# Kernel optimization log

Hardware: AMD Instinct MI355X
Metric: run time of the kernel (lower is better)

Reference implementation:

```python
import jax, jax.numpy as jnp
import numpy as np

D_MODEL = 768
N_HEADS = 12
HEAD_DIM = D_MODEL // N_HEADS
D_FF = 4 * D_MODEL
EPS = 1e-5


def setup_inputs() -> dict:
    key = jax.random.key(0)
    ks = jax.random.split(key, 16)
    s = 0.02
    x = jax.random.normal(ks[0], (2, 2048, D_MODEL), dtype=jnp.float32)
    wq = jax.random.normal(ks[1], (D_MODEL, D_MODEL), dtype=jnp.float32) * s
    bq = jnp.zeros((D_MODEL,), jnp.float32)
    wk = jax.random.normal(ks[2], (D_MODEL, D_MODEL), dtype=jnp.float32) * s
    bk = jnp.zeros((D_MODEL,), jnp.float32)
    wv = jax.random.normal(ks[3], (D_MODEL, D_MODEL), dtype=jnp.float32) * s
    bv = jnp.zeros((D_MODEL,), jnp.float32)
    wo = jax.random.normal(ks[4], (D_MODEL, D_MODEL), dtype=jnp.float32) * s
    bo = jnp.zeros((D_MODEL,), jnp.float32)
    w1 = jax.random.normal(ks[5], (D_MODEL, D_FF), dtype=jnp.float32) * s
    b1 = jnp.zeros((D_FF,), jnp.float32)
    w2 = jax.random.normal(ks[6], (D_FF, D_MODEL), dtype=jnp.float32) * s
    b2 = jnp.zeros((D_MODEL,), jnp.float32)
    ln1_g = jnp.ones((D_MODEL,), jnp.float32)
    ln1_b = jnp.zeros((D_MODEL,), jnp.float32)
    ln2_g = jnp.ones((D_MODEL,), jnp.float32)
    ln2_b = jnp.zeros((D_MODEL,), jnp.float32)
    return dict(x=x, wq=wq, bq=bq, wk=wk, bk=bk, wv=wv, bv=bv, wo=wo, bo=bo,
                w1=w1, b1=b1, w2=w2, b2=b2,
                ln1_g=ln1_g, ln1_b=ln1_b, ln2_g=ln2_g, ln2_b=ln2_b)


def _layernorm(x, g, b):
    mu = jnp.mean(x, axis=-1, keepdims=True)
    var = jnp.mean(jnp.square(x - mu), axis=-1, keepdims=True)
    return (x - mu) * jax.lax.rsqrt(var + EPS) * g + b


def _attention(x, wq, bq, wk, bk, wv, bv, wo, bo):
    B, S, D = x.shape
    def split_heads(t):  # [B,S,D] -> [B,H,S,Hd]
        return t.reshape(B, S, N_HEADS, HEAD_DIM).transpose(0, 2, 1, 3)
    q = split_heads(x @ wq + bq)
    k = split_heads(x @ wk + bk)
    v = split_heads(x @ wv + bv)
    scores = jnp.einsum('bhqd,bhkd->bhqk', q, k) / np.sqrt(HEAD_DIM).astype(np.float32)
    causal = jnp.tril(jnp.ones((S, S), dtype=bool))
    scores = jnp.where(causal, scores, -jnp.inf)
    weights = jax.nn.softmax(scores, axis=-1)
    attn = jnp.einsum('bhqk,bhkd->bhqd', weights, v)
    attn = attn.transpose(0, 2, 1, 3).reshape(B, S, D)
    return attn @ wo + bo


def reference(x, wq, bq, wk, bk, wv, bv, wo, bo, w1, b1, w2, b2,
              ln1_g, ln1_b, ln2_g, ln2_b):
    x = x + _attention(_layernorm(x, ln1_g, ln1_b), wq, bq, wk, bk, wv, bv, wo, bo)
    h = _layernorm(x, ln2_g, ln2_b)
    ff = jax.nn.relu(h @ w1 + b1) @ w2 + b2
    return x + ff
```

## Files before the change

kernel.cpp:

```cpp
#include <hip/hip_runtime.h>
#include <stdint.h>

typedef __bf16 bf16;
typedef float f32x4 __attribute__((ext_vector_type(4)));
typedef bf16 bf16x8 __attribute__((ext_vector_type(8)));
typedef bf16 bf16x4 __attribute__((ext_vector_type(4)));

#define MFMA16(a, b, c) __builtin_amdgcn_mfma_f32_16x16x32_bf16((a), (b), (c), 0, 0, 0)

static __device__ __forceinline__ void load_lds16(const bf16* g, bf16* l) {
  __builtin_amdgcn_global_load_lds(
      (const __attribute__((address_space(1))) void*)g,
      (__attribute__((address_space(3))) void*)l, 16, 0, 0);
}

__global__ void __launch_bounds__(256) k_prep(
    const float* __restrict__ x, const float* __restrict__ ln1g,
    const float* __restrict__ ln1b, bf16* __restrict__ h1,
    const float* s0, const float* s1, const float* s2, const float* s3,
    const float* s4, const float* s5,
    bf16* d0, bf16* d1, bf16* d2, bf16* d3, bf16* d4, bf16* d5) {
  int t = blockIdx.x;
  int tid = threadIdx.x;
  if (t < 6912) {
    const float* src; bf16* dst; int R, C;
    if (t < 2304) {
      int z = t / 576; t -= z * 576;
      src = (z == 0) ? s0 : (z == 1) ? s1 : (z == 2) ? s2 : s3;
      dst = (z == 0) ? d0 : (z == 1) ? d1 : (z == 2) ? d2 : d3;
      R = 768; C = 768;
    } else if (t < 4608) {
      t -= 2304; src = s4; dst = d4; R = 768; C = 3072;
    } else {
      t -= 4608; src = s5; dst = d5; R = 3072; C = 768;
    }
    int tcn = C >> 5;
    int tr = t / tcn, tc = t % tcn;
    __shared__ float tile[32][33];
    int tx = tid & 31, ty = tid >> 5;
    for (int i = 0; i < 4; i++)
      tile[ty + i * 8][tx] = src[(size_t)(tr * 32 + ty + i * 8) * C + tc * 32 + tx];
    __syncthreads();
    for (int i = 0; i < 4; i++)
      dst[(size_t)(tc * 32 + ty + i * 8) * R + tr * 32 + tx] = (bf16)tile[tx][ty + i * 8];
  } else {
    int row = t - 6912;
    const float* rp = x + (size_t)row * 768;
    float v0 = rp[tid], v1 = rp[tid + 256], v2 = rp[tid + 512];
    float s = v0 + v1 + v2, sq = v0 * v0 + v1 * v1 + v2 * v2;
    for (int off = 1; off < 64; off <<= 1) {
      s += __shfl_xor(s, off, 64);
      sq += __shfl_xor(sq, off, 64);
    }
    __shared__ float ps[8];
    if ((tid & 63) == 0) { ps[tid >> 6] = s; ps[4 + (tid >> 6)] = sq; }
    __syncthreads();
    s = ps[0] + ps[1] + ps[2] + ps[3];
    sq = ps[4] + ps[5] + ps[6] + ps[7];
    float mu = s * (1.0f / 768.0f);
    float rstd = rsqrtf(sq * (1.0f / 768.0f) - mu * mu + 1e-5f);
    bf16* op = h1 + (size_t)row * 768;
    op[tid] = (bf16)((v0 - mu) * rstd * ln1g[tid] + ln1b[tid]);
    op[tid + 256] = (bf16)((v1 - mu) * rstd * ln1g[tid + 256] + ln1b[tid + 256]);
    op[tid + 512] = (bf16)((v2 - mu) * rstd * ln1g[tid + 512] + ln1b[tid + 512]);
  }
}

__global__ void __launch_bounds__(256) k_ln2_reduce(
    const float* __restrict__ p0, const float* __restrict__ p1,
    const float* __restrict__ x, const float* __restrict__ bo,
    const float* __restrict__ gam, const float* __restrict__ bet,
    float* __restrict__ x1, bf16* __restrict__ h2) {
  int row = blockIdx.x, tid = threadIdx.x;
  size_t base = (size_t)row * 768;
  float v0 = p0[base + tid] + p1[base + tid] + x[base + tid] + bo[tid];
  float v1 = p0[base + tid + 256] + p1[base + tid + 256] + x[base + tid + 256] + bo[tid + 256];
  float v2 = p0[base + tid + 512] + p1[base + tid + 512] + x[base + tid + 512] + bo[tid + 512];
  x1[base + tid] = v0; x1[base + tid + 256] = v1; x1[base + tid + 512] = v2;
  float s = v0 + v1 + v2, sq = v0 * v0 + v1 * v1 + v2 * v2;
  for (int off = 1; off < 64; off <<= 1) {
    s += __shfl_xor(s, off, 64);
    sq += __shfl_xor(sq, off, 64);
  }
  __shared__ float ps[8];
  if ((tid & 63) == 0) { ps[tid >> 6] = s; ps[4 + (tid >> 6)] = sq; }
  __syncthreads();
  s = ps[0] + ps[1] + ps[2] + ps[3];
  sq = ps[4] + ps[5] + ps[6] + ps[7];
  float mu = s * (1.0f / 768.0f);
  float rstd = rsqrtf(sq * (1.0f / 768.0f) - mu * mu + 1e-5f);
  bf16* op = h2 + base;
  op[tid] = (bf16)((v0 - mu) * rstd * gam[tid] + bet[tid]);
  op[tid + 256] = (bf16)((v1 - mu) * rstd * gam[tid + 256] + bet[tid + 256]);
  op[tid + 512] = (bf16)((v2 - mu) * rstd * gam[tid + 512] + bet[tid + 512]);
}

__global__ void __launch_bounds__(256) k_ff2_reduce(
    const float* __restrict__ f0, const float* __restrict__ f1,
    const float* __restrict__ f2, const float* __restrict__ f3,
    const float* __restrict__ x1, const float* __restrict__ b2,
    float* __restrict__ out) {
  size_t i = ((size_t)blockIdx.x * 256 + threadIdx.x) * 4;
  int col = (int)(i % 768);
  f32x4 v = *(const f32x4*)(x1 + i);
  f32x4 b = *(const f32x4*)(b2 + col);
  f32x4 a0 = *(const f32x4*)(f0 + i), a1 = *(const f32x4*)(f1 + i);
  f32x4 a2 = *(const f32x4*)(f2 + i), a3 = *(const f32x4*)(f3 + i);
  *(f32x4*)(out + i) = v + b + a0 + a1 + a2 + a3;
}

template <int MT>
static __device__ __forceinline__ void gemm_core(
    const bf16* __restrict__ A, int lda, const bf16* __restrict__ Bt, int ldb,
    int Kc, int m0, int n0, bf16* As, bf16* Bs, f32x4 acc[MT][4]) {
  int tid = threadIdx.x, w = tid >> 6, lane = tid & 63, quad = lane >> 4, l15 = lane & 15;
  int wr = w >> 1, wc = w & 1;
  int srow = lane >> 2, sk = (lane & 3) * 8;
  const int ABUF = MT * 32 * 32;
  const int BBUF = 128 * 32;

  auto stage = [&](int k0, int buf) {
    bf16* Ab = As + buf * ABUF;
    bf16* Bb = Bs + buf * BBUF;
    if (MT == 4) {
      for (int c = 0; c < 2; c++) {
        int seg = w * 2 + c;
        load_lds16(A + (size_t)(m0 + seg * 16 + srow) * lda + k0 + sk, Ab + seg * 512);
      }
    } else {
      load_lds16(A + (size_t)(m0 + w * 16 + srow) * lda + k0 + sk, Ab + w * 512);
    }
    for (int c = 0; c < 2; c++) {
      int seg = w * 2 + c;
      load_lds16(Bt + (size_t)(n0 + seg * 16 + srow) * ldb + k0 + sk, Bb + seg * 512);
    }
  };

  stage(0, 0);
  int cur = 0;
  for (int k0 = 0; k0 < Kc; k0 += 32) {
    __syncthreads();
    if (k0 + 32 < Kc) stage(k0 + 32, cur ^ 1);
    const bf16* Ab = As + cur * ABUF;
    const bf16* Bb = Bs + cur * BBUF;
    bf16x8 af[MT], bfr[4];
    for (int mi = 0; mi < MT; mi++)
      af[mi] = *(const bf16x8*)(Ab + (wr * (MT * 16) + mi * 16 + l15) * 32 + quad * 8);
    for (int ni = 0; ni < 4; ni++)
      bfr[ni] = *(const bf16x8*)(Bb + (wc * 64 + ni * 16 + l15) * 32 + quad * 8);
    for (int mi = 0; mi < MT; mi++)
      for (int ni = 0; ni < 4; ni++)
        acc[mi][ni] = MFMA16(af[mi], bfr[ni], acc[mi][ni]);
    cur ^= 1;
  }
}

template <int MT>
__global__ void __launch_bounds__(256, 3) k_gemm(
    const bf16* __restrict__ A, const bf16* __restrict__ Bt,
    const float* __restrict__ bias, bf16* __restrict__ outp, int K_, int N_) {
  __shared__ __align__(16) bf16 As[2 * MT * 32 * 32];
  __shared__ __align__(16) bf16 Bs[2 * 128 * 32];
  int m0 = blockIdx.y * (MT * 32), n0 = blockIdx.x * 128;
  f32x4 acc[MT][4] = {};
  gemm_core<MT>(A, K_, Bt, K_, K_, m0, n0, As, Bs, acc);
  int tid = threadIdx.x, w = tid >> 6, lane = tid & 63, quad = lane >> 4, l15 = lane & 15;
  int wr = w >> 1, wc = w & 1;
  float bv[4];
  for (int ni = 0; ni < 4; ni++) bv[ni] = bias[n0 + wc * 64 + ni * 16 + l15];
  for (int mi = 0; mi < MT; mi++) {
    int mb = m0 + wr * (MT * 16) + mi * 16 + quad * 4;
    for (int ni = 0; ni < 4; ni++) {
      int n = n0 + wc * 64 + ni * 16 + l15;
      for (int r = 0; r < 4; r++) {
        float val = acc[mi][ni][r] + bv[ni];
        outp[(size_t)(mb + r) * N_ + n] = (bf16)fmaxf(val, 0.0f);
      }
    }
  }
}

template <int MT>
__global__ void __launch_bounds__(256, 3) k_gemm_split(
    const bf16* __restrict__ A, const bf16* __restrict__ Bt,
    float* __restrict__ f0, float* __restrict__ f1,
    float* __restrict__ f2, float* __restrict__ f3, int K_, int Kc, int N_) {
  __shared__ __align__(16) bf16 As[2 * MT * 32 * 32];
  __shared__ __align__(16) bf16 Bs[2 * 128 * 32];
  int z = blockIdx.z;
  float* outp = (z == 0) ? f0 : (z == 1) ? f1 : (z == 2) ? f2 : f3;
  int m0 = blockIdx.y * (MT * 32), n0 = blockIdx.x * 128;
  f32x4 acc[MT][4] = {};
  gemm_core<MT>(A + (size_t)z * Kc, K_, Bt + (size_t)z * Kc, K_, Kc, m0, n0, As, Bs, acc);
  int tid = threadIdx.x, w = tid >> 6, lane = tid & 63, quad = lane >> 4, l15 = lane & 15;
  int wr = w >> 1, wc = w & 1;
  for (int mi = 0; mi < MT; mi++) {
    int mb = m0 + wr * (MT * 16) + mi * 16 + quad * 4;
    for (int ni = 0; ni < 4; ni++) {
      int n = n0 + wc * 64 + ni * 16 + l15;
      for (int r = 0; r < 4; r++)
        outp[(size_t)(mb + r) * N_ + n] = acc[mi][ni][r];
    }
  }
}

template <int MT>
__global__ void __launch_bounds__(256, 3) k_gemm_qkv(
    const bf16* __restrict__ h1, const bf16* __restrict__ wqT,
    const bf16* __restrict__ wkT, const bf16* __restrict__ wvT,
    const float* __restrict__ bq, const float* __restrict__ bk,
    const float* __restrict__ bv, bf16* __restrict__ qb,
    bf16* __restrict__ kb, bf16* __restrict__ vtb) {
  __shared__ __align__(16) bf16 As[2 * MT * 32 * 32];
  __shared__ __align__(16) bf16 Bs[2 * 128 * 32];
  int z = blockIdx.z;
  const bf16* Bt = (z == 0) ? wqT : (z == 1) ? wkT : wvT;
  const float* bias = (z == 0) ? bq : (z == 1) ? bk : bv;
  int m0 = blockIdx.y * (MT * 32), n0 = blockIdx.x * 128;
  f32x4 acc[MT][4] = {};
  gemm_core<MT>(h1, 768, Bt, 768, 768, m0, n0, As, Bs, acc);
  int tid = threadIdx.x, w = tid >> 6, lane = tid & 63, quad = lane >> 4, l15 = lane & 15;
  int wr = w >> 1, wc = w & 1;
  float bvv[4];
  for (int ni = 0; ni < 4; ni++) bvv[ni] = bias[n0 + wc * 64 + ni * 16 + l15];
  for (int mi = 0; mi < MT; mi++) {
    int mb = m0 + wr * (MT * 16) + mi * 16 + quad * 4;
    int b = mb >> 11, s0_ = mb & 2047;
    for (int ni = 0; ni < 4; ni++) {
      int n = n0 + wc * 64 + ni * 16 + l15;
      int h = n >> 6, hd = n & 63;
      if (z < 2) {
        bf16* outp = (z == 0) ? qb : kb;
        size_t base = (size_t)(b * 12 + h) * 2048 * 64;
        for (int r = 0; r < 4; r++)
          outp[base + (size_t)(s0_ + r) * 64 + hd] = (bf16)(acc[mi][ni][r] + bvv[ni]);
      } else {
        bf16x4 pk;
        for (int r = 0; r < 4; r++) pk[r] = (bf16)(acc[mi][ni][r] + bvv[ni]);
        *(bf16x4*)(vtb + (((size_t)(b * 12 + h) * 64 + hd) * 2048 + s0_)) = pk;
      }
    }
  }
}

__global__ void __launch_bounds__(256, 3) k_attn(
    const bf16* __restrict__ qb, const bf16* __restrict__ kb,
    const bf16* __restrict__ vtb, bf16* __restrict__ out) {
  __shared__ __align__(16) bf16 Ks[2 * 128 * 64];
  __shared__ __align__(16) bf16 Vs[64 * 128];
  int g = blockIdx.x / 24;
  int bh = blockIdx.x % 24;
  int qt = (g & 1) ? (g >> 1) : (31 - (g >> 1));
  int q0 = qt * 64;
  int tid = threadIdx.x, w = tid >> 6, lane = tid & 63, quad = lane >> 4, l15 = lane & 15;
  const bf16* qbase = qb + (size_t)bh * 2048 * 64;
  const bf16* kbase = kb + (size_t)bh * 2048 * 64;
  const bf16* vbase = vtb + (size_t)bh * 64 * 2048;

  bf16x8 qf[2];
  for (int ds = 0; ds < 2; ds++)
    qf[ds] = *(const bf16x8*)(qbase + (size_t)(q0 + w * 16 + l15) * 64 + ds * 32 + quad * 8);

  f32x4 o[4] = {};
  f32x4 l_i = {};

  auto stageK = [&](int k0, int buf) {
    int rsub = lane >> 3, c8 = lane & 7;
    bf16* Kb = Ks + buf * (128 * 64);
    for (int c = 0; c < 4; c++) {
      int seg = c * 4 + w;
      int row = seg * 8 + rsub;
      load_lds16(kbase + (size_t)(k0 + row) * 64 + ((c8 ^ (row & 7)) * 8), Kb + seg * 512);
    }
  };
  auto stageV = [&](int k0) {
    int rsub2 = lane >> 4, c16 = lane & 15;
    for (int c = 0; c < 4; c++) {
      int seg = c * 4 + w;
      int row = seg * 4 + rsub2;
      load_lds16(vbase + (size_t)row * 2048 + k0 + ((c16 ^ (row & 15)) * 8), Vs + seg * 512);
    }
  };

  const float C2 = 0.18033688011112042f;
  int nkt = (qt >> 1) + 1;
  stageK(0, 0);
  int cur = 0;
  for (int kt = 0; kt < nkt; kt++) {
    int k0 = kt * 128;
    __syncthreads();
    if (kt + 1 < nkt) stageK(k0 + 128, cur ^ 1);
    stageV(k0);
    const bf16* Kb = Ks + cur * (128 * 64);
    bf16* Pw = Ks + cur * (128 * 64) + w * 2048;

    f32x4 sc[8] = {};
    for (int kj = 0; kj < 8; kj++) {
      int krow = kj * 16 + l15;
      for (int ds = 0; ds < 2; ds++) {
        bf16x8 kf = *(const bf16x8*)(Kb + krow * 64 + (((ds * 4 + quad) ^ (krow & 7)) * 8));
        sc[kj] = MFMA16(qf[ds], kf, sc[kj]);
      }
    }
    if (kt == nkt - 1) {
      int qg = q0 + w * 16 + quad * 4;
      for (int kj = 0; kj < 8; kj++) {
        int kg = k0 + kj * 16 + l15;
        for (int r = 0; r < 4; r++)
          if (kg > qg + r) sc[kj][r] = -3.0e38f;
      }
    }
    f32x4 lsum = {};
    for (int kj = 0; kj < 8; kj++)
      for (int r = 0; r < 4; r++) {
        float p = exp2f(sc[kj][r] * C2);
        sc[kj][r] = p;
        lsum[r] += p;
      }
    for (int off = 1; off < 16; off <<= 1)
      for (int r = 0; r < 4; r++) lsum[r] += __shfl_xor(lsum[r], off, 64);
    for (int r = 0; r < 4; r++) l_i[r] += lsum[r];

    __syncthreads();

    for (int kj = 0; kj < 8; kj++) {
      int colb = kj * 16 + l15;
      int chb = colb >> 3, cin = colb & 7;
      for (int r = 0; r < 4; r++) {
        int prow = quad * 4 + r;
        Pw[prow * 128 + ((chb ^ prow) * 8) + cin] = (bf16)sc[kj][r];
      }
    }
    for (int ks = 0; ks < 4; ks++) {
      int prow = l15;
      bf16x8 pf = *(const bf16x8*)(Pw + prow * 128 + (((ks * 4 + quad) ^ prow) * 8));
      for (int dj = 0; dj < 4; dj++) {
        int vrow = dj * 16 + l15;
        bf16x8 vf = *(const bf16x8*)(Vs + vrow * 128 + (((ks * 4 + quad) ^ (vrow & 15)) * 8));
        o[dj] = MFMA16(pf, vf, o[dj]);
      }
    }
    cur ^= 1;
  }
  int b = bh / 12, h = bh % 12;
  f32x4 rl;
  for (int r = 0; r < 4; r++) rl[r] = 1.0f / l_i[r];
  int srow = q0 + w * 16 + quad * 4;
  for (int dj = 0; dj < 4; dj++) {
    int d = h * 64 + dj * 16 + l15;
    for (int r = 0; r < 4; r++)
      out[(size_t)(b * 2048 + srow + r) * 768 + d] = (bf16)(o[dj][r] * rl[r]);
  }
}

extern "C" void kernel_launch(void* const* d_in, const int* in_sizes, int n_in,
                              void* d_out, int out_size, void* d_ws, size_t ws_size,
                              hipStream_t stream) {
  const float* x    = (const float*)d_in[0];
  const float* wq   = (const float*)d_in[1];
  const float* bq   = (const float*)d_in[2];
  const float* wk   = (const float*)d_in[3];
  const float* bk   = (const float*)d_in[4];
  const float* wv   = (const float*)d_in[5];
  const float* bv   = (const float*)d_in[6];
  const float* wo   = (const float*)d_in[7];
  const float* bo   = (const float*)d_in[8];
  const float* w1   = (const float*)d_in[9];
  const float* b1   = (const float*)d_in[10];
  const float* w2   = (const float*)d_in[11];
  const float* b2   = (const float*)d_in[12];
  const float* ln1g = (const float*)d_in[13];
  const float* ln1b = (const float*)d_in[14];
  const float* ln2g = (const float*)d_in[15];
  const float* ln2b = (const float*)d_in[16];

  char* p = (char*)d_ws;
  bf16* wqT = (bf16*)p; p += (size_t)768 * 768 * 2;
  bf16* wkT = (bf16*)p; p += (size_t)768 * 768 * 2;
  bf16* wvT = (bf16*)p; p += (size_t)768 * 768 * 2;
  bf16* woT = (bf16*)p; p += (size_t)768 * 768 * 2;
  bf16* w1T = (bf16*)p; p += (size_t)768 * 3072 * 2;
  bf16* w2T = (bf16*)p; p += (size_t)768 * 3072 * 2;
  bf16* h1   = (bf16*)p; p += (size_t)4096 * 768 * 2;
  bf16* qbuf = (bf16*)p; p += (size_t)4096 * 768 * 2;
  bf16* kbuf = (bf16*)p; p += (size_t)4096 * 768 * 2;
  bf16* vtb  = (bf16*)p; p += (size_t)4096 * 768 * 2;
  bf16* att  = (bf16*)p; p += (size_t)4096 * 768 * 2;
  float* x1  = (float*)p; p += (size_t)4096 * 768 * 4;
  bf16* h2   = (bf16*)p; p += (size_t)4096 * 768 * 2;
  bf16* ffm  = (bf16*)p; p += (size_t)4096 * 3072 * 2;
  float* p0  = (float*)p; p += (size_t)4096 * 768 * 4;
  float* p1  = (float*)p; p += (size_t)4096 * 768 * 4;
  float* f0 = (float*)h1;
  float* f1 = (float*)kbuf;
  float* f2 = p0;
  float* f3 = p1;

  k_prep<<<dim3(11008), dim3(256), 0, stream>>>(
      x, ln1g, ln1b, h1, wq, wk, wv, wo, w1, w2, wqT, wkT, wvT, woT, w1T, w2T);
  k_gemm_qkv<2><<<dim3(6, 64, 3), dim3(256), 0, stream>>>(
      h1, wqT, wkT, wvT, bq, bk, bv, qbuf, kbuf, vtb);
  k_attn<<<dim3(768), dim3(256), 0, stream>>>(qbuf, kbuf, vtb, att);
  k_gemm_split<2><<<dim3(6, 64, 2), dim3(256), 0, stream>>>(
      att, woT, p0, p1, p0, p1, 768, 384, 768);
  k_ln2_reduce<<<dim3(4096), dim3(256), 0, stream>>>(
      p0, p1, x, bo, ln2g, ln2b, x1, h2);
  k_gemm<4><<<dim3(24, 32), dim3(256), 0, stream>>>(
      h2, w1T, b1, ffm, 768, 3072);
  k_gemm_split<4><<<dim3(6, 32, 4), dim3(256), 0, stream>>>(
      ffm, w2T, f0, f1, f2, f3, 3072, 768, 768);
  k_ff2_reduce<<<dim3(3072), dim3(256), 0, stream>>>(
      f0, f1, f2, f3, x1, b2, (float*)d_out);
}
```

Before: 290.0 us.

## Double-buffer K/V in attention, compute row sums via MFMA, retune QKV tiling

The attention kernel now double-buffers V alongside K and writes P into a dedicated per-wave LDS region. This removes the second __syncthreads per tile. The softmax denominator is accumulated with an extra MFMA against a ones vector instead of cross-lane shuffles. The change also adds s_setprio around the MFMA sections, uses a simple descending-tile block order, and lowers the occupancy hint from 3 to 2. The QKV GEMM switches to a larger M tile with half the grid, trading LDS use and occupancy for less synchronisation and better reuse.

Result: faster. 279.2 us (-3.7%).

```diff
diff --git a/kernel.cpp b/kernel.cpp
--- a/kernel.cpp
+++ b/kernel.cpp
@@ -243,14 +243,14 @@
   }
 }
 
-__global__ void __launch_bounds__(256, 3) k_attn(
+__global__ void __launch_bounds__(256, 2) k_attn(
     const bf16* __restrict__ qb, const bf16* __restrict__ kb,
     const bf16* __restrict__ vtb, bf16* __restrict__ out) {
   __shared__ __align__(16) bf16 Ks[2 * 128 * 64];
-  __shared__ __align__(16) bf16 Vs[64 * 128];
-  int g = blockIdx.x / 24;
+  __shared__ __align__(16) bf16 Vs[2 * 64 * 128];
+  __shared__ __align__(16) bf16 Ps[4][16 * 128];
+  int qt = 31 - (blockIdx.x / 24);
   int bh = blockIdx.x % 24;
-  int qt = (g & 1) ? (g >> 1) : (31 - (g >> 1));
   int q0 = qt * 64;
   int tid = threadIdx.x, w = tid >> 6, lane = tid & 63, quad = lane >> 4, l15 = lane & 15;
   const bf16* qbase = qb + (size_t)bh * 2048 * 64;
@@ -261,10 +261,13 @@
   for (int ds = 0; ds < 2; ds++)
     qf[ds] = *(const bf16x8*)(qbase + (size_t)(q0 + w * 16 + l15) * 64 + ds * 32 + quad * 8);
 
+  bf16 one_ = (bf16)1.0f;
+  bf16x8 ones8 = {one_, one_, one_, one_, one_, one_, one_, one_};
+
   f32x4 o[4] = {};
-  f32x4 l_i = {};
-
-  auto stageK = [&](int k0, int buf) {
+  f32x4 lacc = {};
+
+  auto stageKV = [&](int k0, int buf) {
     int rsub = lane >> 3, c8 = lane & 7;
     bf16* Kb = Ks + buf * (128 * 64);
     for (int c = 0; c < 4; c++) {
@@ -272,29 +275,28 @@
       int row = seg * 8 + rsub;
       load_lds16(kbase + (size_t)(k0 + row) * 64 + ((c8 ^ (row & 7)) * 8), Kb + seg * 512);
     }
-  };
-  auto stageV = [&](int k0) {
     int rsub2 = lane >> 4, c16 = lane & 15;
+    bf16* Vb = Vs + buf * (64 * 128);
     for (int c = 0; c < 4; c++) {
       int seg = c * 4 + w;
       int row = seg * 4 + rsub2;
-      load_lds16(vbase + (size_t)row * 2048 + k0 + ((c16 ^ (row & 15)) * 8), Vs + seg * 512);
+      load_lds16(vbase + (size_t)row * 2048 + k0 + ((c16 ^ (row & 15)) * 8), Vb + seg * 512);
     }
   };
 
   const float C2 = 0.18033688011112042f;
   int nkt = (qt >> 1) + 1;
-  stageK(0, 0);
+  stageKV(0, 0);
   int cur = 0;
   for (int kt = 0; kt < nkt; kt++) {
     int k0 = kt * 128;
     __syncthreads();
-    if (kt + 1 < nkt) stageK(k0 + 128, cur ^ 1);
-    stageV(k0);
+    if (kt + 1 < nkt) stageKV(k0 + 128, cur ^ 1);
     const bf16* Kb = Ks + cur * (128 * 64);
-    bf16* Pw = Ks + cur * (128 * 64) + w * 2048;
+    const bf16* Vb = Vs + cur * (64 * 128);
 
     f32x4 sc[8] = {};
+    __builtin_amdgcn_s_setprio(1);
     for (int kj = 0; kj < 8; kj++) {
       int krow = kj * 16 + l15;
       for (int ds = 0; ds < 2; ds++) {
@@ -302,6 +304,7 @@
         sc[kj] = MFMA16(qf[ds], kf, sc[kj]);
       }
     }
+    __builtin_amdgcn_s_setprio(0);
     if (kt == nkt - 1) {
       int qg = q0 + w * 16 + quad * 4;
       for (int kj = 0; kj < 8; kj++) {
@@ -310,41 +313,34 @@
           if (kg > qg + r) sc[kj][r] = -3.0e38f;
       }
     }
-    f32x4 lsum = {};
     for (int kj = 0; kj < 8; kj++)
-      for (int r = 0; r < 4; r++) {
-        float p = exp2f(sc[kj][r] * C2);
-        sc[kj][r] = p;
-        lsum[r] += p;
-      }
-    for (int off = 1; off < 16; off <<= 1)
-      for (int r = 0; r < 4; r++) lsum[r] += __shfl_xor(lsum[r], off, 64);
-    for (int r = 0; r < 4; r++) l_i[r] += lsum[r];
-
-    __syncthreads();
-
+      for (int r = 0; r < 4; r++)
+        sc[kj][r] = exp2f(sc[kj][r] * C2);
     for (int kj = 0; kj < 8; kj++) {
       int colb = kj * 16 + l15;
       int chb = colb >> 3, cin = colb & 7;
       for (int r = 0; r < 4; r++) {
         int prow = quad * 4 + r;
-        Pw[prow * 128 + ((chb ^ prow) * 8) + cin] = (bf16)sc[kj][r];
-      }
-    }
+        Ps[w][prow * 128 + ((chb ^ prow) * 8) + cin] = (bf16)sc[kj][r];
+      }
+    }
+    __builtin_amdgcn_s_setprio(1);
     for (int ks = 0; ks < 4; ks++) {
       int prow = l15;
-      bf16x8 pf = *(const bf16x8*)(Pw + prow * 128 + (((ks * 4 + quad) ^ prow) * 8));
+      bf16x8 pf = *(const bf16x8*)(&Ps[w][prow * 128 + (((ks * 4 + quad) ^ prow) * 8)]);
+      lacc = MFMA16(pf, ones8, lacc);
       for (int dj = 0; dj < 4; dj++) {
         int vrow = dj * 16 + l15;
-        bf16x8 vf = *(const bf16x8*)(Vs + vrow * 128 + (((ks * 4 + quad) ^ (vrow & 15)) * 8));
+        bf16x8 vf = *(const bf16x8*)(Vb + vrow * 128 + (((ks * 4 + quad) ^ (vrow & 15)) * 8));
         o[dj] = MFMA16(pf, vf, o[dj]);
       }
     }
+    __builtin_amdgcn_s_setprio(0);
     cur ^= 1;
   }
   int b = bh / 12, h = bh % 12;
   f32x4 rl;
-  for (int r = 0; r < 4; r++) rl[r] = 1.0f / l_i[r];
+  for (int r = 0; r < 4; r++) rl[r] = 1.0f / lacc[r];
   int srow = q0 + w * 16 + quad * 4;
   for (int dj = 0; dj < 4; dj++) {
     int d = h * 64 + dj * 16 + l15;
@@ -398,7 +394,7 @@
 
   k_prep<<<dim3(11008), dim3(256), 0, stream>>>(
       x, ln1g, ln1b, h1, wq, wk, wv, wo, w1, w2, wqT, wkT, wvT, woT, w1T, w2T);
-  k_gemm_qkv<2><<<dim3(6, 64, 3), dim3(256), 0, stream>>>(
+  k_gemm_qkv<4><<<dim3(6, 32, 3), dim3(256), 0, stream>>>(
       h1, wqT, wkT, wvT, bq, bk, bv, qbuf, kbuf, vtb);
   k_attn<<<dim3(768), dim3(256), 0, stream>>>(qbuf, kbuf, vtb, att);
   k_gemm_split<2><<<dim3(6, 64, 2), dim3(256), 0, stream>>>(
```
